# Performance work log

Hardware: AMD Instinct MI355X
Metric: run time of the kernel (lower is better)

## Reference

```python
import jax, jax.numpy as jnp
import numpy as np

NUM_HEADS = 32
NUM_KV_HEADS = 8
HEAD_DIM = 128
HIDDEN = 4096
BLOCK_SIZE = 16
NUM_BLOCKS = 512
BLOCKS_PER_REQ = 256
B, S = 1, 2048
ROPE_BASE = 10000.0


def _rope_cos_sin(seq_len, dim, dtype):
    inv_freq = 1.0 / (ROPE_BASE ** (jnp.arange(0, dim, 2, dtype=jnp.float32) / dim))
    t = jnp.arange(seq_len, dtype=jnp.float32)
    freqs = jnp.outer(t, inv_freq)            # [S, dim/2]
    emb = jnp.concatenate([freqs, freqs], -1)  # [S, dim]
    return jnp.cos(emb).astype(dtype), jnp.sin(emb).astype(dtype)


def _rotate_half(x):
    d = x.shape[-1] // 2
    return jnp.concatenate([-x[..., d:], x[..., :d]], axis=-1)


def setup_inputs() -> dict:
    key = jax.random.key(0)
    ks = jax.random.split(key, 6)
    sc = 0.02
    return {
        "hidden_states": jax.random.normal(ks[0], (B, S, HIDDEN), jnp.float32),
        "k_cache": jax.random.normal(ks[1], (NUM_BLOCKS, NUM_KV_HEADS, BLOCK_SIZE, HEAD_DIM), jnp.float32),
        "v_cache": jax.random.normal(ks[2], (NUM_BLOCKS, NUM_KV_HEADS, BLOCK_SIZE, HEAD_DIM), jnp.float32),
        "Wq": jax.random.normal(ks[3], (HIDDEN, HIDDEN), jnp.float32) * sc,
        "Wo": jax.random.normal(ks[4], (HIDDEN, HIDDEN), jnp.float32) * sc,
        "block_table": jax.random.randint(ks[5], (BLOCKS_PER_REQ,), 0, NUM_BLOCKS, jnp.int32),
    }


def reference(hidden_states, k_cache, v_cache, Wq, Wo, block_table):
    Bq, Sq, D = hidden_states.shape
    # query projection + reshape to [B, H, S, d]
    q = (hidden_states @ Wq.T).reshape(Bq, Sq, NUM_HEADS, HEAD_DIM).transpose(0, 2, 1, 3)
    cos, sin = _rope_cos_sin(Sq, HEAD_DIM, q.dtype)  # [S, d]
    q = q * cos[None, None] + _rotate_half(q) * sin[None, None]

    # paged KV gather: [n_blk, kvH, blk, d] -> [kvH, kv_len, d]
    kv_len = BLOCKS_PER_REQ * BLOCK_SIZE
    K = k_cache[block_table].transpose(1, 0, 2, 3).reshape(NUM_KV_HEADS, kv_len, HEAD_DIM)
    V = v_cache[block_table].transpose(1, 0, 2, 3).reshape(NUM_KV_HEADS, kv_len, HEAD_DIM)

    # GQA: repeat_interleave kv heads to q heads
    factor = NUM_HEADS // NUM_KV_HEADS
    K = jnp.repeat(K, factor, axis=0)[None]  # [1, H, kv_len, d]
    V = jnp.repeat(V, factor, axis=0)[None]

    scores = jnp.einsum('bhsd,bhkd->bhsk', q, K) / jnp.sqrt(jnp.asarray(HEAD_DIM, q.dtype))
    attn = jax.nn.softmax(scores, axis=-1)
    ctx = jnp.einsum('bhsk,bhkd->bhsd', attn, V)
    ctx = ctx.transpose(0, 2, 1, 3).reshape(Bq, Sq, D)
    return ctx @ Wo.T
```

## Files before the change

kernel.cpp:

```cpp
#include <hip/hip_runtime.h>
#include <hip/hip_bf16.h>

typedef __bf16 bf16;
typedef __bf16 bf16x4 __attribute__((ext_vector_type(4)));
typedef __bf16 bf16x8 __attribute__((ext_vector_type(8)));
typedef float f32x4 __attribute__((ext_vector_type(4)));

#define AS1 __attribute__((address_space(1)))
#define AS3 __attribute__((address_space(3)))
#define GLD16(gptr, lptr) \
  __builtin_amdgcn_global_load_lds((const AS1 unsigned int*)(gptr), \
                                   (AS3 unsigned int*)(lptr), 16, 0, 0)

#define NUM_H   32
#define NUM_KVH 8
#define DH      128
#define SEQ     2048
#define KVLEN   4096
#define HID     4096
#define RSCALE  0.08838834764831845f

__global__ void prep_hs(const float* __restrict__ hs, bf16* __restrict__ out) {
  int tid = blockIdx.x * 256 + threadIdx.x;
  size_t o = (size_t)tid * 8;
  float4 a = *(const float4*)(hs + o);
  float4 b = *(const float4*)(hs + o + 4);
  bf16x8 w = {(bf16)a.x, (bf16)a.y, (bf16)a.z, (bf16)a.w,
              (bf16)b.x, (bf16)b.y, (bf16)b.z, (bf16)b.w};
  *(bf16x8*)(out + o) = w;
}

__global__ void prep_w2(const float* __restrict__ Wq, const float* __restrict__ Wo,
                        bf16* __restrict__ Qo, bf16* __restrict__ Oo) {
  int half = blockIdx.x & 8191;
  const float* src = (blockIdx.x < 8192) ? Wq : Wo;
  bf16* dst = (blockIdx.x < 8192) ? Qo : Oo;
  int tid = half * 256 + threadIdx.x;
  size_t o = (size_t)tid * 8;
  float4 a = *(const float4*)(src + o);
  float4 b = *(const float4*)(src + o + 4);
  bf16x8 w = {(bf16)a.x, (bf16)a.y, (bf16)a.z, (bf16)a.w,
              (bf16)b.x, (bf16)b.y, (bf16)b.z, (bf16)b.w};
  *(bf16x8*)(dst + o) = w;
}

__global__ void prep_k(const float* __restrict__ kc, const int* __restrict__ bt,
                       bf16* __restrict__ Kg) {
  int tid = blockIdx.x * 256 + threadIdx.x;
  int c   = tid & 31;
  int j   = (tid >> 5) & 4095;
  int kvh = tid >> 17;
  int blk = bt[j >> 4];
  float4 v = *(const float4*)(kc + (((size_t)blk * NUM_KVH + kvh) * 16 + (j & 15)) * DH + c * 4);
  bf16x4 w = {(bf16)v.x, (bf16)v.y, (bf16)v.z, (bf16)v.w};
  *(bf16x4*)(Kg + ((size_t)kvh * KVLEN + j) * DH + c * 4) = w;
}

__global__ void prep_v(const float* __restrict__ vc, const int* __restrict__ bt,
                       bf16* __restrict__ Vt) {
  __shared__ bf16 T[32][136];
  int e2 = blockIdx.x & 127, kvh = blockIdx.x >> 7;
  int t = threadIdx.x;
#pragma unroll
  for (int i = 0; i < 4; i++) {
    int idx = i * 256 + t;
    int pg  = idx >> 9;
    int pos = (idx >> 5) & 15;
    int c4  = idx & 31;
    int blk = bt[e2 * 2 + pg];
    float4 v = *(const float4*)(vc + (((size_t)blk * NUM_KVH + kvh) * 16 + pos) * DH + c4 * 4);
    bf16x4 w = {(bf16)v.x, (bf16)v.y, (bf16)v.z, (bf16)v.w};
    *(bf16x4*)(&T[pg * 16 + pos][c4 * 4]) = w;
  }
  __syncthreads();
  int d = t & 127, jc = t >> 7;
  bf16 tmp[16];
#pragma unroll
  for (int j = 0; j < 16; j++) tmp[j] = T[jc * 16 + j][d];
  bf16* dst = Vt + ((size_t)kvh * DH + d) * KVLEN + e2 * 32 + jc * 16;
  *(bf16x8*)dst = *(bf16x8*)tmp;
  *(bf16x8*)(dst + 8) = *(bf16x8*)(tmp + 8);
}

template <typename CT>
__global__ __launch_bounds__(256, 2)
void gemm_bb(const bf16* __restrict__ A, const bf16* __restrict__ B,
             CT* __restrict__ C, int M, int N, int K) {
  __shared__ alignas(16) bf16 As[2][128 * 64];
  __shared__ alignas(16) bf16 Bs[2][128 * 64];
  const int nwg = gridDim.x;
  const int q8  = nwg >> 3;
  const int wg  = ((int)blockIdx.x & 7) * q8 + ((int)blockIdx.x >> 3);
  const int nb = N >> 7;
  const int bm = wg / nb;
  const int bn = wg % nb;
  const int t = threadIdx.x;
  const int lane = t & 63, wave = t >> 6;
  const int lid = lane & 15, quad = lane >> 4;
  const int wm = (wave >> 1) * 64, wn = (wave & 1) * 64;
  const bf16* Ab = A + (size_t)bm * 128 * K;
  const bf16* Bb = B + (size_t)bn * 128 * K;
  f32x4 acc[4][4] = {};

  auto stage = [&](int buf, int k0) {
#pragma unroll
    for (int i = 0; i < 4; i++) {
      int id = i * 256 + t;
      int row = id >> 3, c = id & 7;
      int gc = c ^ (row & 7);
      GLD16(Ab + (size_t)row * K + k0 + gc * 8, &As[buf][id * 8]);
    }
#pragma unroll
    for (int i = 0; i < 4; i++) {
      int id = i * 256 + t;
      int row = id >> 3, c = id & 7;
      int gc = c ^ (row & 7);
      GLD16(Bb + (size_t)row * K + k0 + gc * 8, &Bs[buf][id * 8]);
    }
  };
  auto compute = [&](int buf) {
#pragma unroll
    for (int kk = 0; kk < 2; kk++) {
      bf16x8 af[4], bfr[4];
#pragma unroll
      for (int i = 0; i < 4; i++) {
        int row = wm + i * 16 + lid;
        af[i] = *(const bf16x8*)(&As[buf][row * 64 + ((kk * 4 + quad) ^ (row & 7)) * 8]);
      }
#pragma unroll
      for (int j = 0; j < 4; j++) {
        int row = wn + j * 16 + lid;
        bfr[j] = *(const bf16x8*)(&Bs[buf][row * 64 + ((kk * 4 + quad) ^ (row & 7)) * 8]);
      }
#pragma unroll
      for (int i = 0; i < 4; i++)
#pragma unroll
        for (int j = 0; j < 4; j++)
          acc[i][j] = __builtin_amdgcn_mfma_f32_16x16x32_bf16(bfr[j], af[i], acc[i][j], 0, 0, 0);
    }
  };

  stage(0, 0);
  int cur = 0;
#pragma unroll 1
  for (int k0 = 64; k0 < K; k0 += 64) {
    stage(cur ^ 1, k0);
    asm volatile("s_waitcnt vmcnt(8)" ::: "memory");
    __builtin_amdgcn_s_barrier();
    __builtin_amdgcn_sched_barrier(0);
    compute(cur);
    __builtin_amdgcn_sched_barrier(0);
    asm volatile("s_waitcnt lgkmcnt(0)" ::: "memory");
    __builtin_amdgcn_s_barrier();
    cur ^= 1;
  }
  asm volatile("s_waitcnt vmcnt(0)" ::: "memory");
  __builtin_amdgcn_s_barrier();
  __builtin_amdgcn_sched_barrier(0);
  compute(cur);

#pragma unroll
  for (int i = 0; i < 4; i++)
#pragma unroll
    for (int j = 0; j < 4; j++) {
      int m = bm * 128 + wm + i * 16 + lid;
      int n = bn * 128 + wn + j * 16 + quad * 4;
      if constexpr (sizeof(CT) == 4) {
        float4 w = {acc[i][j][0], acc[i][j][1], acc[i][j][2], acc[i][j][3]};
        *(float4*)(&C[(size_t)m * N + n]) = w;
      } else {
        bf16x4 w = {(bf16)acc[i][j][0], (bf16)acc[i][j][1],
                    (bf16)acc[i][j][2], (bf16)acc[i][j][3]};
        *(bf16x4*)(&C[(size_t)m * N + n]) = w;
      }
    }
}

__global__ void rope_q(bf16* __restrict__ Q) {
  __shared__ float tcs[64], tsn[64];
  int s = blockIdx.x;
  int t = threadIdx.x;
  if (t < 64) {
    float freq = expf(-(float)t * (logf(10000.f) / 64.f));
    float sn, cs;
    sincosf((float)s * freq, &sn, &cs);
    tsn[t] = sn; tcs[t] = cs;
  }
  __syncthreads();
  int h = t >> 3, d0 = (t & 7) * 8;
  bf16* ptr = Q + (size_t)s * HID + h * DH;
  bf16x8 lo = *(bf16x8*)(ptr + d0);
  bf16x8 hi = *(bf16x8*)(ptr + 64 + d0);
  bf16x8 olo, ohi;
#pragma unroll
  for (int e = 0; e < 8; e++) {
    float cs = tcs[d0 + e], sn = tsn[d0 + e];
    float q0 = (float)lo[e], q1 = (float)hi[e];
    olo[e] = (bf16)((q0 * cs - q1 * sn) * RSCALE);
    ohi[e] = (bf16)((q1 * cs + q0 * sn) * RSCALE);
  }
  *(bf16x8*)(ptr + d0) = olo;
  *(bf16x8*)(ptr + 64 + d0) = ohi;
}

__global__ __launch_bounds__(256, 2)
void attn(bf16* __restrict__ Q,
          const bf16* __restrict__ Kg,
          const bf16* __restrict__ Vt) {
  __shared__ alignas(16) bf16 Ks[2][64 * 128];
  __shared__ alignas(16) bf16 Vs[2][128 * 64];
  __shared__ alignas(16) bf16 Ps[4][2][1024];
  const int bid = ((int)blockIdx.x & 7) * 64 + ((int)blockIdx.x >> 3);
  const int h = bid >> 4, qt2 = bid & 15;
  const int kvh = h >> 2;
  const int t = threadIdx.x;
  const int wave = t >> 6, lane = t & 63;
  const int lid = lane & 15, quad = lane >> 4;

  bf16x8 qf[2][4];
#pragma unroll
  for (int x = 0; x < 2; x++) {
    const bf16* qb = Q + (size_t)(qt2 * 128 + x * 64 + wave * 16 + lid) * HID + h * DH;
#pragma unroll
    for (int kc = 0; kc < 4; kc++) qf[x][kc] = *(const bf16x8*)(qb + kc * 32 + quad * 8);
  }
  const bf16* Kh = Kg + (size_t)kvh * KVLEN * DH;
  const bf16* Vh = Vt + (size_t)kvh * DH * KVLEN;
  f32x4 acc_o[2][8] = {};
  f32x4 lsum[2] = {};
  const bf16 one = (bf16)1.0f;
  const bf16x8 ones = {one, one, one, one, one, one, one, one};

  auto stage = [&](int buf, int kv0) {
#pragma unroll
    for (int i = 0; i < 4; i++) {
      int id = i * 256 + t;
      int row = id >> 4, cs = id & 15;
      int gc = cs ^ (row & 7);
      GLD16(Kh + (size_t)(kv0 + row) * DH + gc * 8, &Ks[buf][id * 8]);
    }
#pragma unroll
    for (int i = 0; i < 4; i++) {
      int id = i * 256 + t;
      int d = id >> 3, cs = id & 7;
      int gc = cs ^ (d & 7);
      GLD16(Vh + (size_t)d * KVLEN + kv0 + gc * 8, &Vs[buf][id * 8]);
    }
  };

  stage(0, 0);
  int cur = 0;
#pragma unroll 1
  for (int kv0 = 0; kv0 < KVLEN; kv0 += 64) {
    if (kv0 + 64 < KVLEN) {
      stage(cur ^ 1, kv0 + 64);
      asm volatile("s_waitcnt vmcnt(8)" ::: "memory");
    } else {
      asm volatile("s_waitcnt vmcnt(0)" ::: "memory");
    }
    __builtin_amdgcn_s_barrier();
    __builtin_amdgcn_sched_barrier(0);

    f32x4 sv[2][4];
#pragma unroll
    for (int n = 0; n < 4; n++) {
      f32x4 s0 = {}, s1 = {};
      int row = n * 16 + lid;
#pragma unroll
      for (int kc = 0; kc < 4; kc++) {
        int cs = (kc * 4 + quad) ^ (row & 7);
        bf16x8 kf = *(const bf16x8*)(&Ks[cur][row * DH + cs * 8]);
        s0 = __builtin_amdgcn_mfma_f32_16x16x32_bf16(kf, qf[0][kc], s0, 0, 0, 0);
        s1 = __builtin_amdgcn_mfma_f32_16x16x32_bf16(kf, qf[1][kc], s1, 0, 0, 0);
      }
      sv[0][n] = s0; sv[1][n] = s1;
    }

#pragma unroll
    for (int x = 0; x < 2; x++)
#pragma unroll
      for (int n = 0; n < 4; n++) {
        bf16x4 w = {(bf16)__expf(sv[x][n][0]), (bf16)__expf(sv[x][n][1]),
                    (bf16)__expf(sv[x][n][2]), (bf16)__expf(sv[x][n][3])};
        int c = (2 * n + (quad >> 1)) ^ (lid & 7);
        *(bf16x4*)(&Ps[wave][x][lid * 64 + c * 8 + (quad & 1) * 4]) = w;
      }

    bf16x8 pf[2][2];
#pragma unroll
    for (int x = 0; x < 2; x++)
#pragma unroll
      for (int kvc = 0; kvc < 2; kvc++) {
        int c = (kvc * 4 + quad) ^ (lid & 7);
        pf[x][kvc] = *(const bf16x8*)(&Ps[wave][x][lid * 64 + c * 8]);
      }

#pragma unroll
    for (int x = 0; x < 2; x++) {
      lsum[x] = __builtin_amdgcn_mfma_f32_16x16x32_bf16(ones, pf[x][0], lsum[x], 0, 0, 0);
      lsum[x] = __builtin_amdgcn_mfma_f32_16x16x32_bf16(ones, pf[x][1], lsum[x], 0, 0, 0);
    }

#pragma unroll
    for (int dt = 0; dt < 8; dt++) {
      int d = dt * 16 + lid;
#pragma unroll
      for (int kvc = 0; kvc < 2; kvc++) {
        int cs = (kvc * 4 + quad) ^ (d & 7);
        bf16x8 vf = *(const bf16x8*)(&Vs[cur][d * 64 + cs * 8]);
        acc_o[0][dt] = __builtin_amdgcn_mfma_f32_16x16x32_bf16(vf, pf[0][kvc], acc_o[0][dt], 0, 0, 0);
        acc_o[1][dt] = __builtin_amdgcn_mfma_f32_16x16x32_bf16(vf, pf[1][kvc], acc_o[1][dt], 0, 0, 0);
      }
    }

    __builtin_amdgcn_sched_barrier(0);
    asm volatile("s_waitcnt lgkmcnt(0)" ::: "memory");
    __builtin_amdgcn_s_barrier();
    cur ^= 1;
  }

#pragma unroll
  for (int x = 0; x < 2; x++) {
    float rinv = 1.0f / lsum[x][0];
    int q = qt2 * 128 + x * 64 + wave * 16 + lid;
#pragma unroll
    for (int dt = 0; dt < 8; dt++) {
      bf16x4 w = {(bf16)(acc_o[x][dt][0] * rinv), (bf16)(acc_o[x][dt][1] * rinv),
                  (bf16)(acc_o[x][dt][2] * rinv), (bf16)(acc_o[x][dt][3] * rinv)};
      *(bf16x4*)(&Q[(size_t)q * HID + h * DH + dt * 16 + quad * 4]) = w;
    }
  }
}

template <typename CT>
__global__ __launch_bounds__(512, 2)
void gemm_bt2(const bf16* __restrict__ A, const float* __restrict__ B,
              CT* __restrict__ C, int M, int N, int K) {
  __shared__ alignas(16) bf16 As[2][128 * 64];
  __shared__ alignas(16) bf16 Bs[2][256 * 64];
  const int nb = N >> 8;
  const int bm = (int)blockIdx.x / nb;
  const int bn = (int)blockIdx.x % nb;
  const int t = threadIdx.x;
  const int lane = t & 63, wave = t >> 6;
  const int lid = lane & 15, quad = lane >> 4;
  const int wm = (wave >> 2) * 64, wn = (wave & 3) * 64;
  const bf16*  Ab = A + (size_t)bm * 128 * K;
  const float* Bb = B + (size_t)bn * 256 * K;
  f32x4 acc[4][4] = {};
  float4 breg[4][2];

  auto issueA = [&](int buf, int k0) {
#pragma unroll
    for (int i = 0; i < 2; i++) {
      int id = i * 512 + t;
      int row = id >> 3, c = id & 7;
      int gc = c ^ (row & 7);
      GLD16(Ab + (size_t)row * K + k0 + gc * 8, &As[buf][id * 8]);
    }
  };
  auto loadB = [&](int k0) {
#pragma unroll
    for (int i = 0; i < 4; i++) {
      int id = i * 512 + t;
      int row = id >> 3, c = id & 7;
      const float* src = Bb + (size_t)row * K + k0 + c * 8;
      breg[i][0] = *(const float4*)(src);
      breg[i][1] = *(const float4*)(src + 4);
    }
  };
  auto writeB = [&](int buf) {
#pragma unroll
    for (int i = 0; i < 4; i++) {
      int id = i * 512 + t;
      int row = id >> 3, c = id & 7;
      int sc = c ^ (row & 7);
      float4 u = breg[i][0], v = breg[i][1];
      bf16x8 w = {(bf16)u.x, (bf16)u.y, (bf16)u.z, (bf16)u.w,
                  (bf16)v.x, (bf16)v.y, (bf16)v.z, (bf16)v.w};
      *(bf16x8*)(&Bs[buf][row * 64 + sc * 8]) = w;
    }
  };
  auto compute = [&](int buf) {
#pragma unroll
    for (int kk = 0; kk < 2; kk++) {
      bf16x8 af[4], bfr[4];
#pragma unroll
      for (int i = 0; i < 4; i++) {
        int row = wm + i * 16 + lid;
        af[i] = *(const bf16x8*)(&As[buf][row * 64 + ((kk * 4 + quad) ^ (row & 7)) * 8]);
      }
#pragma unroll
      for (int j = 0; j < 4; j++) {
        int row = wn + j * 16 + lid;
        bfr[j] = *(const bf16x8*)(&Bs[buf][row * 64 + ((kk * 4 + quad) ^ (row & 7)) * 8]);
      }
#pragma unroll
      for (int i = 0; i < 4; i++)
#pragma unroll
        for (int j = 0; j < 4; j++)
          acc[i][j] = __builtin_amdgcn_mfma_f32_16x16x32_bf16(af[i], bfr[j], acc[i][j], 0, 0, 0);
    }
  };

  issueA(0, 0);
  loadB(0);
  writeB(0);
  __syncthreads();

  int cur = 0;
#pragma unroll 1
  for (int k0 = 64; k0 < K; k0 += 64) {
    issueA(cur ^ 1, k0);
    loadB(k0);
    __builtin_amdgcn_sched_barrier(0);
    compute(cur);
    __builtin_amdgcn_sched_barrier(0);
    writeB(cur ^ 1);
    __syncthreads();
    cur ^= 1;
  }
  compute(cur);

#pragma unroll
  for (int i = 0; i < 4; i++)
#pragma unroll
    for (int j = 0; j < 4; j++)
#pragma unroll
      for (int r = 0; r < 4; r++) {
        int m = bm * 128 + wm + i * 16 + quad * 4 + r;
        int n = bn * 256 + wn + j * 16 + lid;
        C[(size_t)m * N + n] = (CT)acc[i][j][r];
      }
}

extern "C" void kernel_launch(void* const* d_in, const int* in_sizes, int n_in,
                              void* d_out, int out_size, void* d_ws, size_t ws_size,
                              hipStream_t stream) {
  const float* hs  = (const float*)d_in[0];
  const float* kca = (const float*)d_in[1];
  const float* vca = (const float*)d_in[2];
  const float* Wq  = (const float*)d_in[3];
  const float* Wo  = (const float*)d_in[4];
  const int*   bt  = (const int*)d_in[5];
  float* out = (float*)d_out;

  bf16* Qlin  = (bf16*)d_ws;
  bf16* Kg    = (bf16*)d_out;
  bf16* Vt    = (bf16*)((char*)d_out + (8u << 20));
  bf16* hs_bf = (bf16*)((char*)d_out + (16u << 20));

  prep_k<<<4096, 256, 0, stream>>>(kca, bt, Kg);
  prep_v<<<1024, 256, 0, stream>>>(vca, bt, Vt);
  prep_hs<<<4096, 256, 0, stream>>>(hs, hs_bf);

  if (ws_size >= (80u << 20)) {
    bf16* Wq_bf = (bf16*)((char*)d_ws + (16u << 20));
    bf16* Wo_bf = (bf16*)((char*)d_ws + (48u << 20));
    prep_w2<<<16384, 256, 0, stream>>>(Wq, Wo, Wq_bf, Wo_bf);
    gemm_bb<bf16><<<512, 256, 0, stream>>>(hs_bf, Wq_bf, Qlin, SEQ, HID, HID);
    rope_q<<<SEQ, 256, 0, stream>>>(Qlin);
    attn<<<512, 256, 0, stream>>>(Qlin, Kg, Vt);
    gemm_bb<float><<<512, 256, 0, stream>>>(Qlin, Wo_bf, out, SEQ, HID, HID);
  } else {
    gemm_bt2<bf16><<<256, 512, 0, stream>>>(hs_bf, Wq, Qlin, SEQ, HID, HID);
    rope_q<<<SEQ, 256, 0, stream>>>(Qlin);
    attn<<<512, 256, 0, stream>>>(Qlin, Kg, Vt);
    gemm_bt2<float><<<256, 512, 0, stream>>>(Qlin, Wo, out, SEQ, HID, HID);
  }
}
```

Measured before the change: 520.3 us.

## Replace bf16 GEMM with 128x256 tile, 8-wave, split-stage pipelined kernel

The projection GEMM moves from 128x128 tiles with 4 waves to 128x256 tiles with 8 waves (512 threads) and 256 workgroups. The next k-tile's global-to-LDS loads are split into A, B-half0 and B-half1 pieces, each interleaved between MFMA sub-phases with barriers. This is meant to overlap memory loads with MFMA work and raise reuse per loaded A tile. The cost is more LDS per block (96KB), more barriers per iteration, and fewer workgroups. The tile raster order also changes so the M index varies fastest.

```diff
diff --git a/kernel.cpp b/kernel.cpp
--- a/kernel.cpp
+++ b/kernel.cpp
@@ -83,88 +83,132 @@
 }
 
 template <typename CT>
-__global__ __launch_bounds__(256, 2)
-void gemm_bb(const bf16* __restrict__ A, const bf16* __restrict__ B,
+__global__ __launch_bounds__(512, 2)
+void gemm_p4(const bf16* __restrict__ A, const bf16* __restrict__ B,
              CT* __restrict__ C, int M, int N, int K) {
   __shared__ alignas(16) bf16 As[2][128 * 64];
-  __shared__ alignas(16) bf16 Bs[2][128 * 64];
+  __shared__ alignas(16) bf16 Bs[2][256 * 64];
   const int nwg = gridDim.x;
   const int q8  = nwg >> 3;
   const int wg  = ((int)blockIdx.x & 7) * q8 + ((int)blockIdx.x >> 3);
-  const int nb = N >> 7;
-  const int bm = wg / nb;
-  const int bn = wg % nb;
+  const int nm  = M >> 7;
+  const int bn  = wg / nm, bm = wg % nm;
   const int t = threadIdx.x;
   const int lane = t & 63, wave = t >> 6;
   const int lid = lane & 15, quad = lane >> 4;
-  const int wm = (wave >> 1) * 64, wn = (wave & 1) * 64;
+  const int wm = (wave >> 2) * 64, wn = (wave & 3) * 64;
   const bf16* Ab = A + (size_t)bm * 128 * K;
-  const bf16* Bb = B + (size_t)bn * 128 * K;
+  const bf16* Bb = B + (size_t)bn * 256 * K;
   f32x4 acc[4][4] = {};
 
-  auto stage = [&](int buf, int k0) {
-#pragma unroll
-    for (int i = 0; i < 4; i++) {
-      int id = i * 256 + t;
-      int row = id >> 3, c = id & 7;
-      int gc = c ^ (row & 7);
+  auto stageA = [&](int buf, int k0) {
+#pragma unroll
+    for (int i = 0; i < 2; i++) {
+      int id = i * 512 + t;
+      int row = id >> 3, c = id & 7, gc = c ^ (row & 7);
       GLD16(Ab + (size_t)row * K + k0 + gc * 8, &As[buf][id * 8]);
     }
-#pragma unroll
-    for (int i = 0; i < 4; i++) {
-      int id = i * 256 + t;
-      int row = id >> 3, c = id & 7;
-      int gc = c ^ (row & 7);
-      GLD16(Bb + (size_t)row * K + k0 + gc * 8, &Bs[buf][id * 8]);
-    }
-  };
-  auto compute = [&](int buf) {
-#pragma unroll
-    for (int kk = 0; kk < 2; kk++) {
-      bf16x8 af[4], bfr[4];
-#pragma unroll
-      for (int i = 0; i < 4; i++) {
-        int row = wm + i * 16 + lid;
-        af[i] = *(const bf16x8*)(&As[buf][row * 64 + ((kk * 4 + quad) ^ (row & 7)) * 8]);
-      }
-#pragma unroll
-      for (int j = 0; j < 4; j++) {
-        int row = wn + j * 16 + lid;
-        bfr[j] = *(const bf16x8*)(&Bs[buf][row * 64 + ((kk * 4 + quad) ^ (row & 7)) * 8]);
-      }
-#pragma unroll
-      for (int i = 0; i < 4; i++)
-#pragma unroll
-        for (int j = 0; j < 4; j++)
-          acc[i][j] = __builtin_amdgcn_mfma_f32_16x16x32_bf16(bfr[j], af[i], acc[i][j], 0, 0, 0);
-    }
-  };
-
-  stage(0, 0);
+    __builtin_amdgcn_sched_barrier(0);
+  };
+  auto stageB = [&](int buf, int k0, int half) {
+#pragma unroll
+    for (int i = 0; i < 2; i++) {
+      int id = i * 512 + t;
+      int row = half * 128 + (id >> 3), c = id & 7, gc = c ^ (row & 7);
+      GLD16(Bb + (size_t)row * K + k0 + gc * 8, &Bs[buf][half * 8192 + id * 8]);
+    }
+    __builtin_amdgcn_sched_barrier(0);
+  };
+
+  stageA(0, 0); stageB(0, 0, 0); stageB(0, 0, 1);
+
+  const int T = K >> 6;
   int cur = 0;
 #pragma unroll 1
-  for (int k0 = 64; k0 < K; k0 += 64) {
-    stage(cur ^ 1, k0);
-    asm volatile("s_waitcnt vmcnt(8)" ::: "memory");
+  for (int tt = 0; tt < T; tt++) {
+    const int kn = (tt + 1 < T ? tt + 1 : tt) * 64;
+    const int nxt = cur ^ 1;
+    bf16x8 af[4], bfr[2];
+
+    stageA(nxt, kn);
+    asm volatile("s_waitcnt vmcnt(2)" ::: "memory");
     __builtin_amdgcn_s_barrier();
     __builtin_amdgcn_sched_barrier(0);
-    compute(cur);
-    __builtin_amdgcn_sched_barrier(0);
-    asm volatile("s_waitcnt lgkmcnt(0)" ::: "memory");
+#pragma unroll
+    for (int i = 0; i < 4; i++) {
+      int row = wm + i * 16 + lid;
+      af[i] = *(const bf16x8*)(&As[cur][row * 64 + (quad ^ (row & 7)) * 8]);
+    }
+#pragma unroll
+    for (int j = 0; j < 2; j++) {
+      int row = wn + j * 16 + lid;
+      bfr[j] = *(const bf16x8*)(&Bs[cur][row * 64 + (quad ^ (row & 7)) * 8]);
+    }
+#pragma unroll
+    for (int i = 0; i < 4; i++) {
+      acc[i][0] = __builtin_amdgcn_mfma_f32_16x16x32_bf16(bfr[0], af[i], acc[i][0], 0, 0, 0);
+      acc[i][1] = __builtin_amdgcn_mfma_f32_16x16x32_bf16(bfr[1], af[i], acc[i][1], 0, 0, 0);
+    }
+    __builtin_amdgcn_sched_barrier(0);
+
+    stageB(nxt, kn, 0);
     __builtin_amdgcn_s_barrier();
-    cur ^= 1;
-  }
-  asm volatile("s_waitcnt vmcnt(0)" ::: "memory");
-  __builtin_amdgcn_s_barrier();
-  __builtin_amdgcn_sched_barrier(0);
-  compute(cur);
+    __builtin_amdgcn_sched_barrier(0);
+#pragma unroll
+    for (int j = 0; j < 2; j++) {
+      int row = wn + (2 + j) * 16 + lid;
+      bfr[j] = *(const bf16x8*)(&Bs[cur][row * 64 + (quad ^ (row & 7)) * 8]);
+    }
+#pragma unroll
+    for (int i = 0; i < 4; i++) {
+      acc[i][2] = __builtin_amdgcn_mfma_f32_16x16x32_bf16(bfr[0], af[i], acc[i][2], 0, 0, 0);
+      acc[i][3] = __builtin_amdgcn_mfma_f32_16x16x32_bf16(bfr[1], af[i], acc[i][3], 0, 0, 0);
+    }
+    __builtin_amdgcn_sched_barrier(0);
+
+    stageB(nxt, kn, 1);
+    __builtin_amdgcn_s_barrier();
+    __builtin_amdgcn_sched_barrier(0);
+#pragma unroll
+    for (int i = 0; i < 4; i++) {
+      int row = wm + i * 16 + lid;
+      af[i] = *(const bf16x8*)(&As[cur][row * 64 + ((4 + quad) ^ (row & 7)) * 8]);
+    }
+#pragma unroll
+    for (int j = 0; j < 2; j++) {
+      int row = wn + j * 16 + lid;
+      bfr[j] = *(const bf16x8*)(&Bs[cur][row * 64 + ((4 + quad) ^ (row & 7)) * 8]);
+    }
+#pragma unroll
+    for (int i = 0; i < 4; i++) {
+      acc[i][0] = __builtin_amdgcn_mfma_f32_16x16x32_bf16(bfr[0], af[i], acc[i][0], 0, 0, 0);
+      acc[i][1] = __builtin_amdgcn_mfma_f32_16x16x32_bf16(bfr[1], af[i], acc[i][1], 0, 0, 0);
+    }
+    __builtin_amdgcn_sched_barrier(0);
+
+    __builtin_amdgcn_s_barrier();
+    __builtin_amdgcn_sched_barrier(0);
+#pragma unroll
+    for (int j = 0; j < 2; j++) {
+      int row = wn + (2 + j) * 16 + lid;
+      bfr[j] = *(const bf16x8*)(&Bs[cur][row * 64 + ((4 + quad) ^ (row & 7)) * 8]);
+    }
+#pragma unroll
+    for (int i = 0; i < 4; i++) {
+      acc[i][2] = __builtin_amdgcn_mfma_f32_16x16x32_bf16(bfr[0], af[i], acc[i][2], 0, 0, 0);
+      acc[i][3] = __builtin_amdgcn_mfma_f32_16x16x32_bf16(bfr[1], af[i], acc[i][3], 0, 0, 0);
+    }
+    __builtin_amdgcn_sched_barrier(0);
+
+    cur = nxt;
+  }
 
 #pragma unroll
   for (int i = 0; i < 4; i++)
 #pragma unroll
     for (int j = 0; j < 4; j++) {
       int m = bm * 128 + wm + i * 16 + lid;
-      int n = bn * 128 + wn + j * 16 + quad * 4;
+      int n = bn * 256 + wn + j * 16 + quad * 4;
       if constexpr (sizeof(CT) == 4) {
         float4 w = {acc[i][j][0], acc[i][j][1], acc[i][j][2], acc[i][j][3]};
         *(float4*)(&C[(size_t)m * N + n]) = w;
@@ -458,10 +502,10 @@
     bf16* Wq_bf = (bf16*)((char*)d_ws + (16u << 20));
     bf16* Wo_bf = (bf16*)((char*)d_ws + (48u << 20));
     prep_w2<<<16384, 256, 0, stream>>>(Wq, Wo, Wq_bf, Wo_bf);
-    gemm_bb<bf16><<<512, 256, 0, stream>>>(hs_bf, Wq_bf, Qlin, SEQ, HID, HID);
+    gemm_p4<bf16><<<256, 512, 0, stream>>>(hs_bf, Wq_bf, Qlin, SEQ, HID, HID);
     rope_q<<<SEQ, 256, 0, stream>>>(Qlin);
     attn<<<512, 256, 0, stream>>>(Qlin, Kg, Vt);
-    gemm_bb<float><<<512, 256, 0, stream>>>(Qlin, Wo_bf, out, SEQ, HID, HID);
+    gemm_p4<float><<<256, 512, 0, stream>>>(Qlin, Wo_bf, out, SEQ, HID, HID);
   } else {
     gemm_bt2<bf16><<<256, 512, 0, stream>>>(hs_bf, Wq, Qlin, SEQ, HID, HID);
     rope_q<<<SEQ, 256, 0, stream>>>(Qlin);
```

Measured after the change: 586.0 us. +12.6%, slower.
